# Kernel tuning notes

Measured on AMD Instinct MI355X. Metric: run time of the kernel, lower is better.

Reference implementation:

```python
import jax, jax.numpy as jnp
import numpy as np

B, T, V, D = 128, 512, 8000, 256
H = D // 2   # per-direction LSTM hidden
L = 4        # label_dim


def setup_inputs() -> dict:
    key = jax.random.key(0)
    ks = jax.random.split(key, 16)
    s = 0.1
    pad_seq = jax.random.randint(ks[0], (B, T), 0, V)
    lens = jax.random.randint(ks[1], (B,), 1, T + 1)
    lens = lens.at[0].set(T)  # padded length == max(lens), as pad_packed_sequence would give
    emb = (jax.random.normal(ks[2], (V, D)) * s).at[0].set(0.0)  # padding_idx=0
    return {
        "pad_seq": pad_seq, "lens": lens, "emb": emb,
        "W_ih_f": jax.random.normal(ks[3], (4 * H, D)) * s,
        "W_hh_f": jax.random.normal(ks[4], (4 * H, H)) * s,
        "b_ih_f": jax.random.normal(ks[5], (4 * H,)) * s,
        "b_hh_f": jax.random.normal(ks[6], (4 * H,)) * s,
        "W_ih_b": jax.random.normal(ks[7], (4 * H, D)) * s,
        "W_hh_b": jax.random.normal(ks[8], (4 * H, H)) * s,
        "b_ih_b": jax.random.normal(ks[9], (4 * H,)) * s,
        "b_hh_b": jax.random.normal(ks[10], (4 * H,)) * s,
        "W_lab": jax.random.normal(ks[11], (L, D)) * s,
        "b_lab": jax.random.normal(ks[12], (L,)) * s,
        "transitions": jax.random.normal(ks[13], (L, L)),
        "from_BOS": jax.random.normal(ks[14], (L,)),
        "to_EOS": jax.random.normal(ks[15], (L,)),
    }


def _lstm(xs_t, mask_t, Wih, Whh, bih, bhh, reverse):
    """Masked unidirectional LSTM over time-major xs_t [T,B,D]; emulates
    pack_padded_sequence semantics (state frozen and output zeroed at pads)."""
    nb, nh = xs_t.shape[1], Whh.shape[1]

    def step(carry, inp):
        h, c = carry
        x_t, m_t = inp  # [B,D], [B,1] bool
        g = x_t @ Wih.T + bih + h @ Whh.T + bhh
        i, f, gg, o = jnp.split(g, 4, axis=-1)
        c2 = jax.nn.sigmoid(f) * c + jax.nn.sigmoid(i) * jnp.tanh(gg)
        h2 = jax.nn.sigmoid(o) * jnp.tanh(c2)
        h = jnp.where(m_t, h2, h)
        c = jnp.where(m_t, c2, c)
        return (h, c), jnp.where(m_t, h2, 0.0)

    init = (jnp.zeros((nb, nh), xs_t.dtype), jnp.zeros((nb, nh), xs_t.dtype))
    _, ys = jax.lax.scan(step, init, (xs_t, mask_t), reverse=reverse)
    return ys  # [T,B,H]


def reference(pad_seq, lens, emb, W_ih_f, W_hh_f, b_ih_f, b_hh_f,
              W_ih_b, W_hh_b, b_ih_b, b_hh_b, W_lab, b_lab,
              transitions, from_BOS, to_EOS):
    b, t = pad_seq.shape
    x = emb[pad_seq]                       # [B,T,D]
    xs_t = jnp.transpose(x, (1, 0, 2))     # [T,B,D]
    mask_t = (jnp.arange(t)[:, None] < lens[None, :])[:, :, None]  # [T,B,1]

    hf = _lstm(xs_t, mask_t, W_ih_f, W_hh_f, b_ih_f, b_hh_f, reverse=False)
    hb = _lstm(xs_t, mask_t, W_ih_b, W_hh_b, b_ih_b, b_hh_b, reverse=True)
    h = jnp.concatenate([hf, hb], axis=-1)           # [T,B,D]
    scores = h @ W_lab.T + b_lab                     # [T,B,L] emissions

    # --- Viterbi forward pass ---
    best0 = from_BOS[None, :] + scores[0]            # [B,L]

    def vstep(best, inp):
        ti, e = inp                                  # step index, emissions [B,L]
        smat = best[:, :, None] + e[:, None, :] + transitions[None]  # [B,prev,cur]
        valid = (lens > ti)[:, None]
        nb = jnp.where(valid, smat.max(axis=1), best)
        return nb, jnp.argmax(smat, axis=1)          # backtrace [B,L]

    bestT, bt = jax.lax.scan(vstep, best0, (jnp.arange(1, t), scores[1:]))
    final_vec = bestT + to_EOS[None, :]              # [B,L]
    last_lab = jnp.argmax(final_vec, axis=1)         # [B]

    # --- backtrace: label[t] = bt[t][label[t+1]] for t < len-1 ---
    bt_pad = jnp.concatenate([bt, jnp.zeros((1,) + bt.shape[1:], bt.dtype)], axis=0)  # [T,B,L]

    def bstep(cur, inp):
        ti, bt_t = inp
        cand = jnp.take_along_axis(bt_t, cur[:, None], axis=1)[:, 0]
        cur = jnp.where(ti == lens - 1, last_lab,
                        jnp.where(ti < lens - 1, cand, cur))
        return cur, cur

    _, labs = jax.lax.scan(bstep, jnp.zeros((b,), last_lab.dtype),
                           (jnp.arange(t), bt_pad), reverse=True)
    labels = labs.T  # [B,T]
    len_bool = jnp.arange(t)[None, :] < lens[:, None]
    return labels * len_bool
```

## Files before the change

### kernel.cpp

```cpp
#include <hip/hip_runtime.h>
#include <math.h>

#define VOCAB 8000
#define BATCH 128
#define TMAX  512
#define DIM   256
#define HID   128
#define G4    512
#define NCOL  1024

#define BARLDS() asm volatile("s_waitcnt lgkmcnt(0)\n\ts_barrier" ::: "memory")

__device__ __forceinline__ float dpp_xor1(float x) {
  int r = __builtin_amdgcn_update_dpp(0, __builtin_bit_cast(int, x),
                                      0xB1, 0xF, 0xF, true);
  return __builtin_bit_cast(float, r);
}
__device__ __forceinline__ float dpp_xor2(float x) {
  int r = __builtin_amdgcn_update_dpp(0, __builtin_bit_cast(int, x),
                                      0x4E, 0xF, 0xF, true);
  return __builtin_bit_cast(float, r);
}
__device__ __forceinline__ unsigned dpp_xor1u(unsigned x) {
  return (unsigned)__builtin_amdgcn_update_dpp(0, (int)x, 0xB1, 0xF, 0xF, true);
}
__device__ __forceinline__ unsigned dpp_xor2u(unsigned x) {
  return (unsigned)__builtin_amdgcn_update_dpp(0, (int)x, 0x4E, 0xF, 0xF, true);
}
__device__ __forceinline__ float dpp_bc0(float x) {
  int r = __builtin_amdgcn_update_dpp(0, __builtin_bit_cast(int, x),
                                      0x00, 0xF, 0xF, true);
  return __builtin_bit_cast(float, r);
}
__device__ __forceinline__ float dpp_bc1(float x) {
  int r = __builtin_amdgcn_update_dpp(0, __builtin_bit_cast(int, x),
                                      0x55, 0xF, 0xF, true);
  return __builtin_bit_cast(float, r);
}
__device__ __forceinline__ float dpp_bc2(float x) {
  int r = __builtin_amdgcn_update_dpp(0, __builtin_bit_cast(int, x),
                                      0xAA, 0xF, 0xF, true);
  return __builtin_bit_cast(float, r);
}
__device__ __forceinline__ float dpp_bc3(float x) {
  int r = __builtin_amdgcn_update_dpp(0, __builtin_bit_cast(int, x),
                                      0xFF, 0xF, 0xF, true);
  return __builtin_bit_cast(float, r);
}

__global__ __launch_bounds__(256) void embw_gemm(
    const float* __restrict__ emb,
    const float* __restrict__ Wf, const float* __restrict__ Wb,
    const float* __restrict__ bihf, const float* __restrict__ bhhf,
    const float* __restrict__ bihb, const float* __restrict__ bhhb,
    float* __restrict__ embW) {
  __shared__ float As[32][132];
  __shared__ float Bs[32][132];
  const int tid = threadIdx.x;
  const int m0 = blockIdx.x * 128;
  const int n0 = blockIdx.y * 128;
  const int tx = tid & 15, ty = tid >> 4;
  const int lrow = tid >> 1;
  const int lseg = (tid & 1) * 16;
  const float* Wsrc = (n0 < 512) ? Wf : Wb;
  const int nbase = (n0 < 512) ? n0 : (n0 - 512);
  const int gm = m0 + lrow;

  float acc[8][8];
  #pragma unroll
  for (int i = 0; i < 8; ++i)
    #pragma unroll
    for (int jj = 0; jj < 8; ++jj) acc[i][jj] = 0.f;

  float4 la[4], lb[4];
#define LOADT(K0)                                                         \
  { _Pragma("unroll")                                                     \
    for (int qq = 0; qq < 4; ++qq) {                                      \
      la[qq] = make_float4(0.f, 0.f, 0.f, 0.f);                           \
      if (gm < VOCAB)                                                     \
        la[qq] = *(const float4*)(emb + (size_t)gm * 256 + (K0) + lseg + 4 * qq); \
      lb[qq] = *(const float4*)(Wsrc + (size_t)(nbase + lrow) * 256 + (K0) + lseg + 4 * qq); \
    } }

  LOADT(0)
  for (int k0 = 0; k0 < 256; k0 += 32) {
    #pragma unroll
    for (int qq = 0; qq < 4; ++qq) {
      As[lseg + 4*qq + 0][lrow] = la[qq].x;
      As[lseg + 4*qq + 1][lrow] = la[qq].y;
      As[lseg + 4*qq + 2][lrow] = la[qq].z;
      As[lseg + 4*qq + 3][lrow] = la[qq].w;
      Bs[lseg + 4*qq + 0][lrow] = lb[qq].x;
      Bs[lseg + 4*qq + 1][lrow] = lb[qq].y;
      Bs[lseg + 4*qq + 2][lrow] = lb[qq].z;
      Bs[lseg + 4*qq + 3][lrow] = lb[qq].w;
    }
    __syncthreads();
    if (k0 + 32 < 256) LOADT(k0 + 32)
    #pragma unroll
    for (int k = 0; k < 32; ++k) {
      float4 av0 = *(const float4*)&As[k][ty * 8];
      float4 av1 = *(const float4*)&As[k][ty * 8 + 4];
      float4 bv0 = *(const float4*)&Bs[k][tx * 4];
      float4 bv1 = *(const float4*)&Bs[k][64 + tx * 4];
      float a[8]  = {av0.x, av0.y, av0.z, av0.w, av1.x, av1.y, av1.z, av1.w};
      float bb[8] = {bv0.x, bv0.y, bv0.z, bv0.w, bv1.x, bv1.y, bv1.z, bv1.w};
      #pragma unroll
      for (int i = 0; i < 8; ++i)
        #pragma unroll
        for (int jj = 0; jj < 8; ++jj)
          acc[i][jj] += a[i] * bb[jj];
    }
    __syncthreads();
  }
#undef LOADT

  float bias[8];
  #pragma unroll
  for (int jj = 0; jj < 8; ++jj) {
    int n = n0 + ((jj < 4) ? (tx * 4 + jj) : (64 + tx * 4 + (jj - 4)));
    bias[jj] = (n < 512) ? (bihf[n] + bhhf[n]) : (bihb[n - 512] + bhhb[n - 512]);
  }
  #pragma unroll
  for (int i = 0; i < 8; ++i) {
    int gmo = m0 + ty * 8 + i;
    if (gmo >= VOCAB) continue;
    float4 v0 = make_float4(acc[i][0] + bias[0], acc[i][1] + bias[1],
                            acc[i][2] + bias[2], acc[i][3] + bias[3]);
    float4 v1 = make_float4(acc[i][4] + bias[4], acc[i][5] + bias[5],
                            acc[i][6] + bias[6], acc[i][7] + bias[7]);
    *(float4*)(embW + (size_t)gmo * NCOL + n0 + tx * 4) = v0;
    *(float4*)(embW + (size_t)gmo * NCOL + n0 + 64 + tx * 4) = v1;
  }
}

#define REP8(M) M(0) M(1) M(2) M(3) M(4) M(5) M(6) M(7)
#define REP8G(M,G) M(G,0) M(G,1) M(G,2) M(G,3) M(G,4) M(G,5) M(G,6) M(G,7)

__global__ __launch_bounds__(512)
__attribute__((amdgpu_waves_per_eu(2, 2)))
void lstm_rec(
    const int* __restrict__ pad_seq, const int* __restrict__ lens,
    const float* __restrict__ Whh_f, const float* __restrict__ Whh_b,
    const float* __restrict__ embW, const float* __restrict__ W_lab,
    float* __restrict__ e_part) {
  const int dir = blockIdx.x & 1;
  const int b   = blockIdx.x >> 1;
  const int tid = threadIdx.x;
  const int j   = tid >> 2;
  const int q   = tid & 3;
  const int parity = q & 1;
  const int half   = (q >> 1) & 1;

  __shared__ float ring[8][4][36];
  __shared__ float wls[4][132];
  __shared__ int   tok[TMAX];

  tok[tid] = pad_seq[b * TMAX + tid];
  wls[tid >> 7][tid & 127] = W_lab[(tid >> 7) * DIM + dir * HID + (tid & 127)];
  if (tid < 144) ((float*)ring)[tid] = 0.f;

  const int len = lens[b];
  const float* __restrict__ Whh = dir ? Whh_b : Whh_f;

  const float4* wr0 = (const float4*)(Whh + (size_t)(0 * HID + j) * HID + 32 * q);
  const float4* wr1 = (const float4*)(Whh + (size_t)(1 * HID + j) * HID + 32 * q);
  const float4* wr2 = (const float4*)(Whh + (size_t)(2 * HID + j) * HID + 32 * q);
  const float4* wr3 = (const float4*)(Whh + (size_t)(3 * HID + j) * HID + 32 * q);
#define DECLW(G,I)                                                      \
  float w##G##_##I##_0, w##G##_##I##_1, w##G##_##I##_2, w##G##_##I##_3; \
  { float4 t = wr##G[I];                                                \
    w##G##_##I##_0 = t.x; w##G##_##I##_1 = t.y;                         \
    w##G##_##I##_2 = t.z; w##G##_##I##_3 = t.w; }                       \
  asm volatile("" : "+v"(w##G##_##I##_0));                              \
  asm volatile("" : "+v"(w##G##_##I##_1));                              \
  asm volatile("" : "+v"(w##G##_##I##_2));                              \
  asm volatile("" : "+v"(w##G##_##I##_3));
  REP8G(DECLW,0) REP8G(DECLW,1) REP8G(DECLW,2) REP8G(DECLW,3)
#undef DECLW

  float c = 0.f;
  const float ascale = (q == 2) ? 2.f : 1.f;
  const float* __restrict__ ecol = embW + dir * G4 + (q * HID + j);
  float* __restrict__ ep = e_part + (size_t)(dir * BATCH + b) * TMAX * 4;

  __syncthreads();

  float xb0, xb1, xb2, xb3, xb4, xb5, xb6, xb7;
  float yb0, yb1, yb2, yb3, yb4, yb5, yb6, yb7;
#define PREX(r) { const int ss = r; xb##r = 0.f;                        \
    if (ss < len) {                                                     \
      const int tt = dir ? (len - 1 - ss) : ss;                         \
      xb##r = ecol[(size_t)tok[tt] * NCOL]; } }
  REP8(PREX)
#undef PREX
#define PREY(r) { const int ss = nbase + r; yb##r = 0.f;                \
    if (ss < len) {                                                     \
      const int tt = dir ? (len - 1 - ss) : ss;                         \
      yb##r = ecol[(size_t)tok[tt] * NCOL]; } }

#define MACC(G,I)                                         \
    a##G##0 = fmaf(hv##I.x, w##G##_##I##_0, a##G##0);     \
    a##G##1 = fmaf(hv##I.y, w##G##_##I##_1, a##G##1);     \
    a##G##2 = fmaf(hv##I.z, w##G##_##I##_2, a##G##2);     \
    a##G##3 = fmaf(hv##I.w, w##G##_##I##_3, a##G##3);

#define STEP(r, XW)                                                     \
  {                                                                     \
    const float4* h4 = (const float4*)&ring[r][q][0];                   \
    float4 hv0 = h4[0], hv1 = h4[1], hv2 = h4[2], hv3 = h4[3];          \
    float4 hv4 = h4[4], hv5 = h4[5], hv6 = h4[6], hv7 = h4[7];          \
    float a00=0.f,a01=0.f,a02=0.f,a03=0.f;                              \
    float a10=0.f,a11=0.f,a12=0.f,a13=0.f;                              \
    float a20=0.f,a21=0.f,a22=0.f,a23=0.f;                              \
    float a30=0.f,a31=0.f,a32=0.f,a33=0.f;                              \
    REP8G(MACC,0) REP8G(MACC,1) REP8G(MACC,2) REP8G(MACC,3)             \
    const float p0 = (a00+a01)+(a02+a03);                               \
    const float p1 = (a10+a11)+(a12+a13);                               \
    const float p2 = (a20+a21)+(a22+a23);                               \
    const float p3 = (a30+a31)+(a32+a33);                               \
    const float klo = parity ? p1 : p0, slo = parity ? p0 : p1;         \
    const float khi = parity ? p3 : p2, shi = parity ? p2 : p3;         \
    const float alo = klo + dpp_xor1(slo);                              \
    const float ahi = khi + dpp_xor1(shi);                              \
    const float kb = half ? ahi : alo, sb = half ? alo : ahi;           \
    const float tot = kb + dpp_xor2(sb);                                \
    const float aa = tot + (XW);                                        \
    const float sg = 1.f / (1.f + __expf(-ascale * aa));                \
    const float act = (q == 2) ? (2.f * sg - 1.f) : sg;                 \
    const float e1 = dpp_xor1(act);                                     \
    const float e2 = dpp_xor2(act);                                     \
    const float e3 = dpp_xor2(e1);                                      \
    const float ev  = parity ? e1 : act, od  = parity ? act : e1;       \
    const float ev2 = parity ? e3 : e2,  od2 = parity ? e2 : e3;        \
    const float ig = half ? ev2 : ev, fg = half ? od2 : od;             \
    const float gt = half ? ev : ev2, og = half ? od : od2;             \
    c = fg * c + ig * gt;                                               \
    const float s2 = 1.f / (1.f + __expf(-2.f * c));                    \
    const float hh = og * (2.f * s2 - 1.f);                             \
    if (q == 0) ring[(r + 1) & 7][j >> 5][j & 31] = hh;                 \
    BARLDS();                                                           \
  }

  for (int s0 = 0; s0 < len; s0 += 8) {
    const int cnt = (len - s0 < 8) ? (len - s0) : 8;
    STEP(0, xb0)
    if (cnt > 1) STEP(1, xb1)
    if (cnt > 2) STEP(2, xb2)
    if (cnt > 3) STEP(3, xb3)
    { const int nbase = s0 + 8; REP8(PREY) }
    if (cnt > 4) STEP(4, xb4)
    if (cnt > 5) STEP(5, xb5)
    if (cnt > 6) STEP(6, xb6)
    if (cnt > 7) STEP(7, xb7)
    {
      const int r = tid >> 6, l = (tid >> 4) & 3, sub = tid & 15;
      if (r < cnt) {
        const float4* hp = (const float4*)&ring[(r + 1) & 7][sub >> 2][8 * (sub & 3)];
        const float4 h0 = hp[0], h1 = hp[1];
        const float4* wp = (const float4*)&wls[l][8 * sub];
        const float4 u0 = wp[0], u1 = wp[1];
        float d = h0.x*u0.x + h0.y*u0.y + h0.z*u0.z + h0.w*u0.w
                + h1.x*u1.x + h1.y*u1.y + h1.z*u1.z + h1.w*u1.w;
        d += __shfl_xor(d, 1); d += __shfl_xor(d, 2);
        d += __shfl_xor(d, 4); d += __shfl_xor(d, 8);
        if (sub == 0) {
          const int ss = s0 + r;
          const int tt = dir ? (len - 1 - ss) : ss;
          ep[tt * 4 + l] = d;
        }
      }
    }
    BARLDS();
    xb0 = yb0; xb1 = yb1; xb2 = yb2; xb3 = yb3;
    xb4 = yb4; xb5 = yb5; xb6 = yb6; xb7 = yb7;
  }
#undef STEP
#undef MACC
#undef PREY
}

__global__ __launch_bounds__(512) void viterbi_k(
    const int* __restrict__ lens, const float* __restrict__ e_part,
    const float* __restrict__ b_lab, const float* __restrict__ trans,
    const float* __restrict__ from_BOS, const float* __restrict__ to_EOS,
    int* __restrict__ out) {
  const int b = blockIdx.x;
  const int tid = threadIdx.x;
  __shared__ float sc[TMAX][4];
  __shared__ unsigned btm[TMAX];
  __shared__ int labs[TMAX];
  const int len = lens[b];

  if (tid < len) {
    const float4 f  = *(const float4*)(e_part + ((size_t)b * TMAX + tid) * 4);
    const float4 g2 = *(const float4*)(e_part + ((size_t)(BATCH + b) * TMAX + tid) * 4);
    const float4 bl = *(const float4*)b_lab;
    sc[tid][0] = f.x + g2.x + bl.x;
    sc[tid][1] = f.y + g2.y + bl.y;
    sc[tid][2] = f.z + g2.z + bl.z;
    sc[tid][3] = f.w + g2.w + bl.w;
  }
  __syncthreads();

  if (tid < 4) {
    const int l = tid;
    float trc0 = trans[0 * 4 + l], trc1 = trans[1 * 4 + l];
    float trc2 = trans[2 * 4 + l], trc3 = trans[3 * 4 + l];
    float best = from_BOS[l] + sc[0][l];
    float eA = sc[(1 < TMAX) ? 1 : 0][l];
    float eB = sc[(2 < TMAX) ? 2 : 0][l];
    float eC = sc[(3 < TMAX) ? 3 : 0][l];
    for (int ti = 1; ti < len; ++ti) {
      const float e = eA;
      eA = eB; eB = eC;
      int nx = ti + 3; if (nx > TMAX - 1) nx = TMAX - 1;
      eC = sc[nx][l];
      const float b0 = dpp_bc0(best);
      const float b1 = dpp_bc1(best);
      const float b2 = dpp_bc2(best);
      const float b3 = dpp_bc3(best);
      float m = (b0 + e) + trc0; int arg = 0;
      float v;
      v = (b1 + e) + trc1; if (v > m) { m = v; arg = 1; }
      v = (b2 + e) + trc2; if (v > m) { m = v; arg = 2; }
      v = (b3 + e) + trc3; if (v > m) { m = v; arg = 3; }
      best = m;
      unsigned av = ((unsigned)arg) << (8 * l);
      av |= dpp_xor1u(av);
      av |= dpp_xor2u(av);
      if (l == 0) btm[ti] = av;
    }
    const float f0 = dpp_bc0(best) + to_EOS[0];
    const float f1 = dpp_bc1(best) + to_EOS[1];
    const float f2 = dpp_bc2(best) + to_EOS[2];
    const float f3 = dpp_bc3(best) + to_EOS[3];
    if (l == 0) {
      float m = f0; int last = 0;
      if (f1 > m) { m = f1; last = 1; }
      if (f2 > m) { m = f2; last = 2; }
      if (f3 > m) { m = f3; last = 3; }
      labs[len - 1] = last;
      int cur = last;
      int ti = len - 2;
      while (ti >= 0) {
        const int hi = ti + 1;
        const unsigned u0 = btm[hi];
        const unsigned u1 = (hi - 1 >= 1) ? btm[hi - 1] : 0u;
        const unsigned u2 = (hi - 2 >= 1) ? btm[hi - 2] : 0u;
        const unsigned u3 = (hi - 3 >= 1) ? btm[hi - 3] : 0u;
        const unsigned u4 = (hi - 4 >= 1) ? btm[hi - 4] : 0u;
        const unsigned u5 = (hi - 5 >= 1) ? btm[hi - 5] : 0u;
        const unsigned u6 = (hi - 6 >= 1) ? btm[hi - 6] : 0u;
        const unsigned u7 = (hi - 7 >= 1) ? btm[hi - 7] : 0u;
        cur = (int)((u0 >> (8 * cur)) & 255u); labs[ti--] = cur; if (ti < 0) break;
        cur = (int)((u1 >> (8 * cur)) & 255u); labs[ti--] = cur; if (ti < 0) break;
        cur = (int)((u2 >> (8 * cur)) & 255u); labs[ti--] = cur; if (ti < 0) break;
        cur = (int)((u3 >> (8 * cur)) & 255u); labs[ti--] = cur; if (ti < 0) break;
        cur = (int)((u4 >> (8 * cur)) & 255u); labs[ti--] = cur; if (ti < 0) break;
        cur = (int)((u5 >> (8 * cur)) & 255u); labs[ti--] = cur; if (ti < 0) break;
        cur = (int)((u6 >> (8 * cur)) & 255u); labs[ti--] = cur; if (ti < 0) break;
        cur = (int)((u7 >> (8 * cur)) & 255u); labs[ti--] = cur;
      }
    }
  }
  __syncthreads();
  out[b * TMAX + tid] = (tid < len) ? labs[tid] : 0;
}

extern "C" void kernel_launch(void* const* d_in, const int* in_sizes, int n_in,
                              void* d_out, int out_size, void* d_ws, size_t ws_size,
                              hipStream_t stream) {
  const int*   pad_seq  = (const int*)d_in[0];
  const int*   lens     = (const int*)d_in[1];
  const float* emb      = (const float*)d_in[2];
  const float* W_ih_f   = (const float*)d_in[3];
  const float* W_hh_f   = (const float*)d_in[4];
  const float* b_ih_f   = (const float*)d_in[5];
  const float* b_hh_f   = (const float*)d_in[6];
  const float* W_ih_b   = (const float*)d_in[7];
  const float* W_hh_b   = (const float*)d_in[8];
  const float* b_ih_b   = (const float*)d_in[9];
  const float* b_hh_b   = (const float*)d_in[10];
  const float* W_lab    = (const float*)d_in[11];
  const float* b_lab    = (const float*)d_in[12];
  const float* trans    = (const float*)d_in[13];
  const float* from_BOS = (const float*)d_in[14];
  const float* to_EOS   = (const float*)d_in[15];
  int* out = (int*)d_out;

  float* embW   = (float*)d_ws;
  float* e_part = embW + (size_t)VOCAB * NCOL;

  embw_gemm<<<dim3(63, 8), 256, 0, stream>>>(emb, W_ih_f, W_ih_b,
                                             b_ih_f, b_hh_f, b_ih_b, b_hh_b, embW);
  lstm_rec<<<dim3(2 * BATCH), 512, 0, stream>>>(pad_seq, lens, W_hh_f, W_hh_b,
                                                embW, W_lab, e_part);
  viterbi_k<<<dim3(BATCH), 512, 0, stream>>>(lens, e_part, b_lab, trans,
                                             from_BOS, to_EOS, out);
}
```

Measured before the change: 585.9 us.

## Split LSTM recurrence over 1024 threads with 8 lanes per hidden unit

Each hidden unit's recurrent dot products are now split across 8 lanes instead of 4, and the block size doubles to 1024 threads. This halves the per-thread register-resident W_hh slice and the serial FMA chain per step, at the cost of an extra cross-lane shuffle reduction and a larger barrier. The input-projection prefetch becomes a rolling per-step reload instead of a double-buffered batch of 8, and the emission dot product is respread over the larger block.

```diff
diff --git a/kernel.cpp b/kernel.cpp
--- a/kernel.cpp
+++ b/kernel.cpp
@@ -135,10 +135,10 @@
 }
 
 #define REP8(M) M(0) M(1) M(2) M(3) M(4) M(5) M(6) M(7)
-#define REP8G(M,G) M(G,0) M(G,1) M(G,2) M(G,3) M(G,4) M(G,5) M(G,6) M(G,7)
-
-__global__ __launch_bounds__(512)
-__attribute__((amdgpu_waves_per_eu(2, 2)))
+#define REP4I(M,G) M(G,0) M(G,1) M(G,2) M(G,3)
+
+__global__ __launch_bounds__(1024)
+__attribute__((amdgpu_waves_per_eu(4, 4)))
 void lstm_rec(
     const int* __restrict__ pad_seq, const int* __restrict__ lens,
     const float* __restrict__ Whh_f, const float* __restrict__ Whh_b,
@@ -147,26 +147,31 @@
   const int dir = blockIdx.x & 1;
   const int b   = blockIdx.x >> 1;
   const int tid = threadIdx.x;
-  const int j   = tid >> 2;
-  const int q   = tid & 3;
-  const int parity = q & 1;
-  const int half   = (q >> 1) & 1;
-
-  __shared__ float ring[8][4][36];
+  const int j   = tid >> 3;
+  const int o   = tid & 7;
+  const int mg  = o & 3;
+  const int parity = o & 1;
+  const int half   = (o >> 1) & 1;
+
+  __shared__ float ring[8][8][36];
   __shared__ float wls[4][132];
   __shared__ int   tok[TMAX];
 
-  tok[tid] = pad_seq[b * TMAX + tid];
-  wls[tid >> 7][tid & 127] = W_lab[(tid >> 7) * DIM + dir * HID + (tid & 127)];
-  if (tid < 144) ((float*)ring)[tid] = 0.f;
+  if (tid < TMAX) {
+    tok[tid] = pad_seq[b * TMAX + tid];
+  } else {
+    const int k2 = tid - TMAX;
+    wls[k2 >> 7][k2 & 127] = W_lab[(k2 >> 7) * DIM + dir * HID + (k2 & 127)];
+  }
+  if (tid < 288) ((float*)ring)[tid] = 0.f;
 
   const int len = lens[b];
   const float* __restrict__ Whh = dir ? Whh_b : Whh_f;
 
-  const float4* wr0 = (const float4*)(Whh + (size_t)(0 * HID + j) * HID + 32 * q);
-  const float4* wr1 = (const float4*)(Whh + (size_t)(1 * HID + j) * HID + 32 * q);
-  const float4* wr2 = (const float4*)(Whh + (size_t)(2 * HID + j) * HID + 32 * q);
-  const float4* wr3 = (const float4*)(Whh + (size_t)(3 * HID + j) * HID + 32 * q);
+  const float4* wr0 = (const float4*)(Whh + (size_t)(0 * HID + j) * HID + 16 * o);
+  const float4* wr1 = (const float4*)(Whh + (size_t)(1 * HID + j) * HID + 16 * o);
+  const float4* wr2 = (const float4*)(Whh + (size_t)(2 * HID + j) * HID + 16 * o);
+  const float4* wr3 = (const float4*)(Whh + (size_t)(3 * HID + j) * HID + 16 * o);
 #define DECLW(G,I)                                                      \
   float w##G##_##I##_0, w##G##_##I##_1, w##G##_##I##_2, w##G##_##I##_3; \
   { float4 t = wr##G[I];                                                \
@@ -176,28 +181,24 @@
   asm volatile("" : "+v"(w##G##_##I##_1));                              \
   asm volatile("" : "+v"(w##G##_##I##_2));                              \
   asm volatile("" : "+v"(w##G##_##I##_3));
-  REP8G(DECLW,0) REP8G(DECLW,1) REP8G(DECLW,2) REP8G(DECLW,3)
+  REP4I(DECLW,0) REP4I(DECLW,1) REP4I(DECLW,2) REP4I(DECLW,3)
 #undef DECLW
 
   float c = 0.f;
-  const float ascale = (q == 2) ? 2.f : 1.f;
-  const float* __restrict__ ecol = embW + dir * G4 + (q * HID + j);
+  const float ascale = (mg == 2) ? 2.f : 1.f;
+  const float* __restrict__ ecol = embW + dir * G4 + (mg * HID + j);
   float* __restrict__ ep = e_part + (size_t)(dir * BATCH + b) * TMAX * 4;
 
   __syncthreads();
 
   float xb0, xb1, xb2, xb3, xb4, xb5, xb6, xb7;
-  float yb0, yb1, yb2, yb3, yb4, yb5, yb6, yb7;
-#define PREX(r) { const int ss = r; xb##r = 0.f;                        \
-    if (ss < len) {                                                     \
+#define PRE(r) { const int ss = nbase + r; xb##r = 0.f;                 \
+    if (o < 4 && ss < len) {                                            \
       const int tt = dir ? (len - 1 - ss) : ss;                         \
-      xb##r = ecol[(size_t)tok[tt] * NCOL]; } }
-  REP8(PREX)
-#undef PREX
-#define PREY(r) { const int ss = nbase + r; yb##r = 0.f;                \
-    if (ss < len) {                                                     \
-      const int tt = dir ? (len - 1 - ss) : ss;                         \
-      yb##r = ecol[(size_t)tok[tt] * NCOL]; } }
+      xb##r = ecol[(size_t)tok[tt] * NCOL]; }                           \
+    asm volatile("" : "+v"(xb##r)); }
+  { const int nbase = 0; REP8(PRE) }
+#define REL(r) { const int nbase = s0 + 8; PRE(r) }
 
 #define MACC(G,I)                                         \
     a##G##0 = fmaf(hv##I.x, w##G##_##I##_0, a##G##0);     \
@@ -207,27 +208,33 @@
 
 #define STEP(r, XW)                                                     \
   {                                                                     \
-    const float4* h4 = (const float4*)&ring[r][q][0];                   \
+    const float4* h4 = (const float4*)&ring[r][o][0];                   \
     float4 hv0 = h4[0], hv1 = h4[1], hv2 = h4[2], hv3 = h4[3];          \
-    float4 hv4 = h4[4], hv5 = h4[5], hv6 = h4[6], hv7 = h4[7];          \
     float a00=0.f,a01=0.f,a02=0.f,a03=0.f;                              \
     float a10=0.f,a11=0.f,a12=0.f,a13=0.f;                              \
     float a20=0.f,a21=0.f,a22=0.f,a23=0.f;                              \
     float a30=0.f,a31=0.f,a32=0.f,a33=0.f;                              \
-    REP8G(MACC,0) REP8G(MACC,1) REP8G(MACC,2) REP8G(MACC,3)             \
-    const float p0 = (a00+a01)+(a02+a03);                               \
-    const float p1 = (a10+a11)+(a12+a13);                               \
-    const float p2 = (a20+a21)+(a22+a23);                               \
-    const float p3 = (a30+a31)+(a32+a33);                               \
+    REP4I(MACC,0) REP4I(MACC,1) REP4I(MACC,2) REP4I(MACC,3)             \
+    float p0 = (a00+a01)+(a02+a03);                                     \
+    float p1 = (a10+a11)+(a12+a13);                                     \
+    float p2 = (a20+a21)+(a22+a23);                                     \
+    float p3 = (a30+a31)+(a32+a33);                                     \
+       \
+    p0 += (o == 0) ? (XW) : 0.f;                                        \
+    p1 += (o == 1) ? (XW) : 0.f;                                        \
+    p2 += (o == 2) ? (XW) : 0.f;                                        \
+    p3 += (o == 3) ? (XW) : 0.f;                                        \
+     \
     const float klo = parity ? p1 : p0, slo = parity ? p0 : p1;         \
     const float khi = parity ? p3 : p2, shi = parity ? p2 : p3;         \
     const float alo = klo + dpp_xor1(slo);                              \
     const float ahi = khi + dpp_xor1(shi);                              \
     const float kb = half ? ahi : alo, sb = half ? alo : ahi;           \
-    const float tot = kb + dpp_xor2(sb);                                \
-    const float aa = tot + (XW);                                        \
-    const float sg = 1.f / (1.f + __expf(-ascale * aa));                \
-    const float act = (q == 2) ? (2.f * sg - 1.f) : sg;                 \
+    const float qs = kb + dpp_xor2(sb);                                 \
+                  \
+    const float tot = qs + __shfl_xor(qs, 4);                           \
+    const float sg = 1.f / (1.f + __expf(-ascale * tot));               \
+    const float act = (mg == 2) ? (2.f * sg - 1.f) : sg;                \
     const float e1 = dpp_xor1(act);                                     \
     const float e2 = dpp_xor2(act);                                     \
     const float e3 = dpp_xor2(e1);                                      \
@@ -238,32 +245,29 @@
     c = fg * c + ig * gt;                                               \
     const float s2 = 1.f / (1.f + __expf(-2.f * c));                    \
     const float hh = og * (2.f * s2 - 1.f);                             \
-    if (q == 0) ring[(r + 1) & 7][j >> 5][j & 31] = hh;                 \
+    if (o == 0) ring[(r + 1) & 7][j >> 4][j & 15] = hh;                 \
     BARLDS();                                                           \
   }
 
   for (int s0 = 0; s0 < len; s0 += 8) {
     const int cnt = (len - s0 < 8) ? (len - s0) : 8;
-    STEP(0, xb0)
-    if (cnt > 1) STEP(1, xb1)
-    if (cnt > 2) STEP(2, xb2)
-    if (cnt > 3) STEP(3, xb3)
-    { const int nbase = s0 + 8; REP8(PREY) }
-    if (cnt > 4) STEP(4, xb4)
-    if (cnt > 5) STEP(5, xb5)
-    if (cnt > 6) STEP(6, xb6)
-    if (cnt > 7) STEP(7, xb7)
+    STEP(0, xb0)  REL(0)
+    if (cnt > 1) { STEP(1, xb1) REL(1) }
+    if (cnt > 2) { STEP(2, xb2) REL(2) }
+    if (cnt > 3) { STEP(3, xb3) REL(3) }
+    if (cnt > 4) { STEP(4, xb4) REL(4) }
+    if (cnt > 5) { STEP(5, xb5) REL(5) }
+    if (cnt > 6) { STEP(6, xb6) REL(6) }
+    if (cnt > 7) { STEP(7, xb7) REL(7) }
     {
-      const int r = tid >> 6, l = (tid >> 4) & 3, sub = tid & 15;
+      const int r = tid >> 7, l = (tid >> 5) & 3, sub = tid & 31;
       if (r < cnt) {
-        const float4* hp = (const float4*)&ring[(r + 1) & 7][sub >> 2][8 * (sub & 3)];
-        const float4 h0 = hp[0], h1 = hp[1];
-        const float4* wp = (const float4*)&wls[l][8 * sub];
-        const float4 u0 = wp[0], u1 = wp[1];
-        float d = h0.x*u0.x + h0.y*u0.y + h0.z*u0.z + h0.w*u0.w
-                + h1.x*u1.x + h1.y*u1.y + h1.z*u1.z + h1.w*u1.w;
+        const float4 h0 = *(const float4*)&ring[(r + 1) & 7][sub >> 2][(sub & 3) * 4];
+        const float4 u0 = *(const float4*)&wls[l][sub * 4];
+        float d = h0.x*u0.x + h0.y*u0.y + h0.z*u0.z + h0.w*u0.w;
         d += __shfl_xor(d, 1); d += __shfl_xor(d, 2);
         d += __shfl_xor(d, 4); d += __shfl_xor(d, 8);
+        d += __shfl_xor(d, 16);
         if (sub == 0) {
           const int ss = s0 + r;
           const int tt = dir ? (len - 1 - ss) : ss;
@@ -272,12 +276,11 @@
       }
     }
     BARLDS();
-    xb0 = yb0; xb1 = yb1; xb2 = yb2; xb3 = yb3;
-    xb4 = yb4; xb5 = yb5; xb6 = yb6; xb7 = yb7;
   }
 #undef STEP
 #undef MACC
-#undef PREY
+#undef REL
+#undef PRE
 }
 
 __global__ __launch_bounds__(512) void viterbi_k(
@@ -394,8 +397,8 @@
 
   embw_gemm<<<dim3(63, 8), 256, 0, stream>>>(emb, W_ih_f, W_ih_b,
                                              b_ih_f, b_hh_f, b_ih_b, b_hh_b, embW);
-  lstm_rec<<<dim3(2 * BATCH), 512, 0, stream>>>(pad_seq, lens, W_hh_f, W_hh_b,
-                                                embW, W_lab, e_part);
+  lstm_rec<<<dim3(2 * BATCH), 1024, 0, stream>>>(pad_seq, lens, W_hh_f, W_hh_b,
+                                                 embW, W_lab, e_part);
   viterbi_k<<<dim3(BATCH), 512, 0, stream>>>(lens, e_part, b_lab, trans,
                                              from_BOS, to_EOS, out);
 }
```

Result: slower. 795.5 us (+35.8%).
